# Optimization experiments

Measured on AMD Instinct MI355X. Metric: run time of the kernel, lower is better.

Reference implementation:

```python
import jax, jax.numpy as jnp
import numpy as np


def setup_inputs() -> dict:
    key = jax.random.key(0)
    k1, k2, k3 = jax.random.split(key, 3)
    N, C, Nf, W, H = 8, 256, 16, 28, 28
    l = jax.random.normal(k1, (N, C, Nf, W, H), dtype=jnp.float32)
    g = jax.random.normal(k2, (N, C, 1, 1, 1), dtype=jnp.float32)
    # 1x1x1 Conv3d(in=C, out=1, bias=False) weight collapses to a length-C vector
    w = jax.random.normal(k3, (C,), dtype=jnp.float32) * (1.0 / np.sqrt(C))
    return {"l": l, "g": g, "w": w}


def reference(l, g, w):
    # l: [N,C,Nf,W,H], g broadcastable to l, w: [C]
    N, C, Nf, W, H = l.shape
    # compatibility score: channel dot-product (1x1x1 conv, out_channels=1)
    c = jnp.einsum('ncfwh,c->nfwh', l + g, w)                      # [N,Nf,W,H]
    # softmax over the spatial dims (W*H) per frame, normalize_attn=True
    a = jax.nn.softmax(c.reshape(N, Nf, W * H), axis=-1)           # [N,Nf,WH]
    a = a.reshape(N, Nf, W, H)
    # attention-weighted spatial sum pooling -> [N,C,Nf]
    g_out = jnp.einsum('nfwh,ncfwh->ncf', a, l)
    # module returns raw compatibility map (pre-softmax) squeezed, and pooled g
    return (c, g_out)
```

## Files before the change

kernel.cpp:

```cpp
#include <hip/hip_runtime.h>
#include <math.h>

constexpr int N_ = 8, C_ = 256, F_ = 16, WH_ = 784;
constexpr int CH_STRIDE = F_ * WH_;
constexpr int COUT_SZ = N_ * F_ * WH_;
constexpr int QP = 392;
constexpr int TILE = 56;
constexpr int NT = 7;
constexpr int F4PT = TILE / 4;
constexpr int TILE_F = C_ * TILE;
constexpr int SOFF = 256 * C_;

__device__ inline float wave_reduce_sum(float v) {
#pragma unroll
  for (int o = 32; o > 0; o >>= 1) v += __shfl_down(v, o, 64);
  return v;
}

__device__ inline void gload16(const float* gp, float* lp) {
  __builtin_amdgcn_global_load_lds(
      (const __attribute__((address_space(1))) void*)gp,
      (__attribute__((address_space(3))) void*)lp, 16, 0, 0);
}

__global__ __launch_bounds__(1024, 4) void fused_kernel(
    const float* __restrict__ l, const float* __restrict__ g,
    const float* __restrict__ w, float* __restrict__ out,
    float* __restrict__ ws) {
  extern __shared__ float dbuf[];
  __shared__ float w_s[C_];
  __shared__ float e_s[TILE];
  __shared__ float red_s[16];
  __shared__ float gb_s;

  const int bid = blockIdx.x;
  const int nf = bid >> 1, half = bid & 1;
  const int n = nf >> 4, f = nf & 15;
  const int tid = threadIdx.x;
  const int lane = tid & 63, wv = tid >> 6;

  int og[4];
#pragma unroll
  for (int k = 0; k < 4; ++k) {
    const int idx = k * 1024 + tid;
    const int c = idx / F4PT, j = idx - c * F4PT;
    og[k] = c * CH_STRIDE + (j << 2);
  }
  const bool a3 = (wv < 8);
  const size_t gbase =
      (size_t)n * (C_ * CH_STRIDE) + (size_t)f * WH_ + half * QP;

  float* cur = dbuf;
  float* nxt = dbuf + TILE_F;

  {
    const float* lp = l + gbase;
    gload16(lp + og[0], &cur[wv << 8]);
    gload16(lp + og[1], &cur[4096 + (wv << 8)]);
    gload16(lp + og[2], &cur[8192 + (wv << 8)]);
    if (a3) gload16(lp + og[3], &cur[12288 + (wv << 8)]);
  }

  if (tid < C_) w_s[tid] = w[tid];
  float gv = (tid < C_) ? g[n * C_ + tid] * w[tid] : 0.f;
  gv = wave_reduce_sum(gv);
  if (lane == 0) red_s[wv] = gv;
  __syncthreads();
  if (tid == 0) {
    float s = 0.f;
#pragma unroll
    for (int i = 0; i < 16; ++i) s += red_s[i];
    gb_s = s;
  }
  __syncthreads();
  const float gb = gb_s;

  const int p16 = tid >> 4, s16 = tid & 15;
  const int gc = tid >> 2, q = tid & 3;

  float gacc = 0.f;
  float s_part = 0.f;

  for (int t = 0; t < NT; ++t) {
    if (t + 1 < NT) {
      const float* lp = l + gbase + (t + 1) * TILE;
      gload16(lp + og[0], &nxt[wv << 8]);
      gload16(lp + og[1], &nxt[4096 + (wv << 8)]);
      gload16(lp + og[2], &nxt[8192 + (wv << 8)]);
      if (a3) gload16(lp + og[3], &nxt[12288 + (wv << 8)]);
    }

    if (tid < TILE * 16) {
      float acc = 0.f;
#pragma unroll
      for (int k = 0; k < 16; ++k) {
        const int c = s16 + (k << 4);
        acc = fmaf(cur[c * TILE + p16], w_s[c], acc);
      }
      acc += __shfl_down(acc, 8, 64);
      acc += __shfl_down(acc, 4, 64);
      acc += __shfl_down(acc, 2, 64);
      acc += __shfl_down(acc, 1, 64);
      if (s16 == 0) {
        const float cp = acc + gb;
        out[nf * WH_ + half * QP + t * TILE + p16] = cp;
        const float e = __expf(cp);
        e_s[p16] = e;
        s_part += e;
      }
    }
    asm volatile("s_waitcnt lgkmcnt(0)" ::: "memory");
    __builtin_amdgcn_s_barrier();
    __builtin_amdgcn_sched_barrier(0);

    {
      const int pb = q * F4PT;
#pragma unroll
      for (int j = 0; j < 14; ++j)
        gacc = fmaf(cur[gc * TILE + pb + j], e_s[pb + j], gacc);
    }
    __syncthreads();

    float* tmp = cur; cur = nxt; nxt = tmp;
  }

  gacc += __shfl_down(gacc, 2, 64);
  gacc += __shfl_down(gacc, 1, 64);
  if (q == 0) ws[bid * C_ + gc] = gacc;

  float sp = wave_reduce_sum(s_part);
  if (lane == 0) red_s[wv] = sp;
  __syncthreads();
  if (tid == 0) {
    float ssum = 0.f;
#pragma unroll
    for (int i = 0; i < 16; ++i) ssum += red_s[i];
    ws[SOFF + bid] = ssum;
  }
}

__global__ __launch_bounds__(1024) void combine_kernel(
    float* __restrict__ out, const float* __restrict__ ws) {
  const int tg = blockIdx.x * 1024 + threadIdx.x;
  const int nf = tg >> 8, c = tg & 255;
  const int n = nf >> 4, f = nf & 15;
  const int b0 = nf << 1;
  const float G = ws[(b0 + 0) * C_ + c] + ws[(b0 + 1) * C_ + c];
  const float S = ws[SOFF + b0] + ws[SOFF + b0 + 1];
  out[COUT_SZ + (size_t)(n * C_ + c) * F_ + f] = G / S;
}

extern "C" void kernel_launch(void* const* d_in, const int* in_sizes, int n_in,
                              void* d_out, int out_size, void* d_ws,
                              size_t ws_size, hipStream_t stream) {
  const float* l = (const float*)d_in[0];
  const float* g = (const float*)d_in[1];
  const float* w = (const float*)d_in[2];
  float* out = (float*)d_out;
  float* ws = (float*)d_ws;
  fused_kernel<<<dim3(2 * N_ * F_), dim3(1024), 2 * TILE_F * sizeof(float),
                 stream>>>(l, g, w, out, ws);
  combine_kernel<<<dim3(32), dim3(1024), 0, stream>>>(out, ws);
}
```

Measured before the change: 158.1 us.

## Stage tiles through registers into padded LDS instead of direct global-to-LDS loads

Replaces the global_load_lds direct-to-LDS prefetch with register-staged float4 global loads. These are written into a padded LDS layout (row stride 60 instead of 56) after the current tile's compute. The padding aims to reduce LDS bank conflicts in the column-strided dot-product and pooling reads. In exchange it uses more registers and LDS, and adds explicit LDS store instructions. The global load latency is now hidden only by the compute that sits between the load and the store.

```diff
diff --git a/kernel.cpp b/kernel.cpp
--- a/kernel.cpp
+++ b/kernel.cpp
@@ -8,19 +8,14 @@
 constexpr int TILE = 56;
 constexpr int NT = 7;
 constexpr int F4PT = TILE / 4;
-constexpr int TILE_F = C_ * TILE;
+constexpr int LSTR = 60;
+constexpr int BUF_F = C_ * LSTR;
 constexpr int SOFF = 256 * C_;
 
 __device__ inline float wave_reduce_sum(float v) {
 #pragma unroll
   for (int o = 32; o > 0; o >>= 1) v += __shfl_down(v, o, 64);
   return v;
-}
-
-__device__ inline void gload16(const float* gp, float* lp) {
-  __builtin_amdgcn_global_load_lds(
-      (const __attribute__((address_space(1))) void*)gp,
-      (__attribute__((address_space(3))) void*)lp, 16, 0, 0);
 }
 
 __global__ __launch_bounds__(1024, 4) void fused_kernel(
@@ -39,32 +34,38 @@
   const int tid = threadIdx.x;
   const int lane = tid & 63, wv = tid >> 6;
 
-  int og[4];
-#pragma unroll
-  for (int k = 0; k < 4; ++k) {
-    const int idx = k * 1024 + tid;
-    const int c = idx / F4PT, j = idx - c * F4PT;
-    og[k] = c * CH_STRIDE + (j << 2);
-  }
-  const bool a3 = (wv < 8);
+  const int c0 = (tid) / F4PT,        j0 = (tid) - c0 * F4PT;
+  const int c1 = (1024 + tid) / F4PT, j1 = (1024 + tid) - c1 * F4PT;
+  const int c2 = (2048 + tid) / F4PT, j2 = (2048 + tid) - c2 * F4PT;
+  const int c3 = (3072 + tid) / F4PT, j3 = (3072 + tid) - c3 * F4PT;
+  const int og0 = c0 * CH_STRIDE + (j0 << 2), ol0 = c0 * LSTR + (j0 << 2);
+  const int og1 = c1 * CH_STRIDE + (j1 << 2), ol1 = c1 * LSTR + (j1 << 2);
+  const int og2 = c2 * CH_STRIDE + (j2 << 2), ol2 = c2 * LSTR + (j2 << 2);
+  const int og3 = c3 * CH_STRIDE + (j3 << 2), ol3 = c3 * LSTR + (j3 << 2);
+  const bool a3 = (tid < 512);
   const size_t gbase =
       (size_t)n * (C_ * CH_STRIDE) + (size_t)f * WH_ + half * QP;
 
   float* cur = dbuf;
-  float* nxt = dbuf + TILE_F;
+  float* nxt = dbuf + BUF_F;
 
+  float4 st0, st1, st2, st3;
   {
     const float* lp = l + gbase;
-    gload16(lp + og[0], &cur[wv << 8]);
-    gload16(lp + og[1], &cur[4096 + (wv << 8)]);
-    gload16(lp + og[2], &cur[8192 + (wv << 8)]);
-    if (a3) gload16(lp + og[3], &cur[12288 + (wv << 8)]);
+    st0 = *reinterpret_cast<const float4*>(lp + og0);
+    st1 = *reinterpret_cast<const float4*>(lp + og1);
+    st2 = *reinterpret_cast<const float4*>(lp + og2);
+    if (a3) st3 = *reinterpret_cast<const float4*>(lp + og3);
   }
 
   if (tid < C_) w_s[tid] = w[tid];
   float gv = (tid < C_) ? g[n * C_ + tid] * w[tid] : 0.f;
   gv = wave_reduce_sum(gv);
   if (lane == 0) red_s[wv] = gv;
+  *reinterpret_cast<float4*>(&cur[ol0]) = st0;
+  *reinterpret_cast<float4*>(&cur[ol1]) = st1;
+  *reinterpret_cast<float4*>(&cur[ol2]) = st2;
+  if (a3) *reinterpret_cast<float4*>(&cur[ol3]) = st3;
   __syncthreads();
   if (tid == 0) {
     float s = 0.f;
@@ -82,12 +83,13 @@
   float s_part = 0.f;
 
   for (int t = 0; t < NT; ++t) {
-    if (t + 1 < NT) {
+    const bool pf = (t + 1 < NT);
+    if (pf) {
       const float* lp = l + gbase + (t + 1) * TILE;
-      gload16(lp + og[0], &nxt[wv << 8]);
-      gload16(lp + og[1], &nxt[4096 + (wv << 8)]);
-      gload16(lp + og[2], &nxt[8192 + (wv << 8)]);
-      if (a3) gload16(lp + og[3], &nxt[12288 + (wv << 8)]);
+      st0 = *reinterpret_cast<const float4*>(lp + og0);
+      st1 = *reinterpret_cast<const float4*>(lp + og1);
+      st2 = *reinterpret_cast<const float4*>(lp + og2);
+      if (a3) st3 = *reinterpret_cast<const float4*>(lp + og3);
     }
 
     if (tid < TILE * 16) {
@@ -95,7 +97,7 @@
 #pragma unroll
       for (int k = 0; k < 16; ++k) {
         const int c = s16 + (k << 4);
-        acc = fmaf(cur[c * TILE + p16], w_s[c], acc);
+        acc = fmaf(cur[c * LSTR + p16], w_s[c], acc);
       }
       acc += __shfl_down(acc, 8, 64);
       acc += __shfl_down(acc, 4, 64);
@@ -117,7 +119,14 @@
       const int pb = q * F4PT;
 #pragma unroll
       for (int j = 0; j < 14; ++j)
-        gacc = fmaf(cur[gc * TILE + pb + j], e_s[pb + j], gacc);
+        gacc = fmaf(cur[gc * LSTR + pb + j], e_s[pb + j], gacc);
+    }
+
+    if (pf) {
+      *reinterpret_cast<float4*>(&nxt[ol0]) = st0;
+      *reinterpret_cast<float4*>(&nxt[ol1]) = st1;
+      *reinterpret_cast<float4*>(&nxt[ol2]) = st2;
+      if (a3) *reinterpret_cast<float4*>(&nxt[ol3]) = st3;
     }
     __syncthreads();
 
@@ -158,7 +167,7 @@
   const float* w = (const float*)d_in[2];
   float* out = (float*)d_out;
   float* ws = (float*)d_ws;
-  fused_kernel<<<dim3(2 * N_ * F_), dim3(1024), 2 * TILE_F * sizeof(float),
+  fused_kernel<<<dim3(2 * N_ * F_), dim3(1024), 2 * BUF_F * sizeof(float),
                  stream>>>(l, g, w, out, ws);
   combine_kernel<<<dim3(32), dim3(1024), 0, stream>>>(out, ws);
 }
```

Result: no change. 160.0 us (+1.2%).

## Triple-buffer smaller tiles with explicit vmcnt waits and deferred score stores

Applied to the files above, without the earlier changes.

Halves the tile width to 28 columns and switches from double to triple buffering, so each global-to-LDS prefetch runs two tiles ahead. Explicit vmcnt waits replace the implicit full drain, letting loads for later tiles stay in flight while the current tile is computed. Compatibility scores are kept in LDS and written to global memory once at the end instead of per tile. In exchange there are more loop iterations and barriers, and the hand-written vmcnt counts must exactly match the number of outstanding loads.

```diff
diff --git a/kernel.cpp b/kernel.cpp
--- a/kernel.cpp
+++ b/kernel.cpp
@@ -5,8 +5,8 @@
 constexpr int CH_STRIDE = F_ * WH_;
 constexpr int COUT_SZ = N_ * F_ * WH_;
 constexpr int QP = 392;
-constexpr int TILE = 56;
-constexpr int NT = 7;
+constexpr int TILE = 28;
+constexpr int NT = 14;
 constexpr int F4PT = TILE / 4;
 constexpr int TILE_F = C_ * TILE;
 constexpr int SOFF = 256 * C_;
@@ -23,6 +23,45 @@
       (__attribute__((address_space(3))) void*)lp, 16, 0, 0);
 }
 
+#define TILE_BODY(T, CUR, VMWAIT)                                            \
+  do {                                                                       \
+    if ((T) + 2 < NT && stg) {                                               \
+      const float* lp_ = l + gbase + ((T) + 2) * TILE;                       \
+      gload16(lp_ + ogA, nx2 + ldsA);                                        \
+      gload16(lp_ + ogB, nx2 + ldsB);                                        \
+    }                                                                        \
+    asm volatile(VMWAIT ::: "memory");                                       \
+    __builtin_amdgcn_s_barrier();                                            \
+    __builtin_amdgcn_sched_barrier(0);                                       \
+    if (tid < TILE * 16) {     \
+      float acc = 0.f;                                                       \
+      _Pragma("unroll") for (int k = 0; k < 16; ++k) {                       \
+        const int c_ = s16 + (k << 4);                                       \
+        acc = fmaf((CUR)[c_ * TILE + p16], w_s[c_], acc);                    \
+      }                                                                      \
+      acc += __shfl_down(acc, 8, 64);                                        \
+      acc += __shfl_down(acc, 4, 64);                                        \
+      acc += __shfl_down(acc, 2, 64);                                        \
+      acc += __shfl_down(acc, 1, 64);                                        \
+      if (s16 == 0) {                                                        \
+        const float cp = acc + gb;                                           \
+        c_save[(T) * TILE + p16] = cp;                                       \
+        const float e_ = __expf(cp);                                         \
+        e_s[p16] = e_;                                                       \
+        s_part += e_;                                                        \
+      }                                                                      \
+    }                                                                        \
+    asm volatile("s_waitcnt lgkmcnt(0)" ::: "memory");                       \
+    __builtin_amdgcn_s_barrier();                                            \
+    __builtin_amdgcn_sched_barrier(0);                                       \
+    {           \
+      _Pragma("unroll") for (int j = 0; j < F4PT; ++j)                       \
+        gacc = fmaf((CUR)[gc * TILE + pbq + j], e_s[pbq + j], gacc);         \
+    }                                                                        \
+    asm volatile("s_waitcnt lgkmcnt(0)" ::: "memory");                       \
+    __builtin_amdgcn_s_barrier();                                            \
+  } while (0)
+
 __global__ __launch_bounds__(1024, 4) void fused_kernel(
     const float* __restrict__ l, const float* __restrict__ g,
     const float* __restrict__ w, float* __restrict__ out,
@@ -30,6 +69,7 @@
   extern __shared__ float dbuf[];
   __shared__ float w_s[C_];
   __shared__ float e_s[TILE];
+  __shared__ float c_save[QP];
   __shared__ float red_s[16];
   __shared__ float gb_s;
 
@@ -39,90 +79,68 @@
   const int tid = threadIdx.x;
   const int lane = tid & 63, wv = tid >> 6;
 
-  int og[4];
-#pragma unroll
-  for (int k = 0; k < 4; ++k) {
-    const int idx = k * 1024 + tid;
-    const int c = idx / F4PT, j = idx - c * F4PT;
-    og[k] = c * CH_STRIDE + (j << 2);
-  }
-  const bool a3 = (wv < 8);
   const size_t gbase =
       (size_t)n * (C_ * CH_STRIDE) + (size_t)f * WH_ + half * QP;
 
-  float* cur = dbuf;
-  float* nxt = dbuf + TILE_F;
+  const bool stg = (tid < 896);
+  const int cA = tid / F4PT, jA = tid - cA * F4PT;
+  const int ogA = cA * CH_STRIDE + (jA << 2);
+  const int sB = 896 + tid;
+  const int cB = sB / F4PT, jB = sB - cB * F4PT;
+  const int ogB = cB * CH_STRIDE + (jB << 2);
+  const int ldsA = wv << 8;
+  const int ldsB = 3584 + (wv << 8);
 
-  {
-    const float* lp = l + gbase;
-    gload16(lp + og[0], &cur[wv << 8]);
-    gload16(lp + og[1], &cur[4096 + (wv << 8)]);
-    gload16(lp + og[2], &cur[8192 + (wv << 8)]);
-    if (a3) gload16(lp + og[3], &cur[12288 + (wv << 8)]);
+  float* b0 = dbuf;
+  float* b1 = dbuf + TILE_F;
+  float* b2 = dbuf + 2 * TILE_F;
+
+  const float wreg = (tid < C_) ? w[tid] : 0.f;
+  const float greg = (tid < C_) ? g[n * C_ + tid] : 0.f;
+  if (stg) {
+    const float* lp0 = l + gbase;
+    gload16(lp0 + ogA, b0 + ldsA);
+    gload16(lp0 + ogB, b0 + ldsB);
+    const float* lp1 = l + gbase + TILE;
+    gload16(lp1 + ogA, b1 + ldsA);
+    gload16(lp1 + ogB, b1 + ldsB);
   }
 
-  if (tid < C_) w_s[tid] = w[tid];
-  float gv = (tid < C_) ? g[n * C_ + tid] * w[tid] : 0.f;
+  if (tid < C_) w_s[tid] = wreg;
+  float gv = wreg * greg;
   gv = wave_reduce_sum(gv);
   if (lane == 0) red_s[wv] = gv;
-  __syncthreads();
+  asm volatile("s_waitcnt lgkmcnt(0)" ::: "memory");
+  __builtin_amdgcn_s_barrier();
   if (tid == 0) {
     float s = 0.f;
 #pragma unroll
     for (int i = 0; i < 16; ++i) s += red_s[i];
     gb_s = s;
   }
-  __syncthreads();
+  asm volatile("s_waitcnt lgkmcnt(0)" ::: "memory");
+  __builtin_amdgcn_s_barrier();
   const float gb = gb_s;
 
   const int p16 = tid >> 4, s16 = tid & 15;
   const int gc = tid >> 2, q = tid & 3;
+  const int pbq = q * F4PT;
 
   float gacc = 0.f;
   float s_part = 0.f;
 
-  for (int t = 0; t < NT; ++t) {
-    if (t + 1 < NT) {
-      const float* lp = l + gbase + (t + 1) * TILE;
-      gload16(lp + og[0], &nxt[wv << 8]);
-      gload16(lp + og[1], &nxt[4096 + (wv << 8)]);
-      gload16(lp + og[2], &nxt[8192 + (wv << 8)]);
-      if (a3) gload16(lp + og[3], &nxt[12288 + (wv << 8)]);
-    }
+  float* cur = b0;
+  float* nx1 = b1;
+  float* nx2 = b2;
 
-    if (tid < TILE * 16) {
-      float acc = 0.f;
-#pragma unroll
-      for (int k = 0; k < 16; ++k) {
-        const int c = s16 + (k << 4);
-        acc = fmaf(cur[c * TILE + p16], w_s[c], acc);
-      }
-      acc += __shfl_down(acc, 8, 64);
-      acc += __shfl_down(acc, 4, 64);
-      acc += __shfl_down(acc, 2, 64);
-      acc += __shfl_down(acc, 1, 64);
-      if (s16 == 0) {
-        const float cp = acc + gb;
-        out[nf * WH_ + half * QP + t * TILE + p16] = cp;
-        const float e = __expf(cp);
-        e_s[p16] = e;
-        s_part += e;
-      }
-    }
-    asm volatile("s_waitcnt lgkmcnt(0)" ::: "memory");
-    __builtin_amdgcn_s_barrier();
-    __builtin_amdgcn_sched_barrier(0);
-
-    {
-      const int pb = q * F4PT;
-#pragma unroll
-      for (int j = 0; j < 14; ++j)
-        gacc = fmaf(cur[gc * TILE + pb + j], e_s[pb + j], gacc);
-    }
-    __syncthreads();
-
-    float* tmp = cur; cur = nxt; nxt = tmp;
+#pragma unroll 1
+  for (int t = 0; t < NT - 2; ++t) {
+    TILE_BODY(t, cur, "s_waitcnt vmcnt(4)");
+    float* tmp = cur; cur = nx1; nx1 = nx2; nx2 = tmp;
   }
+  TILE_BODY(NT - 2, cur, "s_waitcnt vmcnt(2)");
+  { float* tmp = cur; cur = nx1; nx1 = nx2; nx2 = tmp; }
+  TILE_BODY(NT - 1, cur, "s_waitcnt vmcnt(0)");
 
   gacc += __shfl_down(gacc, 2, 64);
   gacc += __shfl_down(gacc, 1, 64);
@@ -137,6 +155,7 @@
     for (int i = 0; i < 16; ++i) ssum += red_s[i];
     ws[SOFF + bid] = ssum;
   }
+  if (tid < QP) out[nf * WH_ + half * QP + tid] = c_save[tid];
 }
 
 __global__ __launch_bounds__(1024) void combine_kernel(
@@ -158,7 +177,7 @@
   const float* w = (const float*)d_in[2];
   float* out = (float*)d_out;
   float* ws = (float*)d_ws;
-  fused_kernel<<<dim3(2 * N_ * F_), dim3(1024), 2 * TILE_F * sizeof(float),
+  fused_kernel<<<dim3(2 * N_ * F_), dim3(1024), 3 * TILE_F * sizeof(float),
                  stream>>>(l, g, w, out, ws);
   combine_kernel<<<dim3(32), dim3(1024), 0, stream>>>(out, ws);
 }
```

Result: no change. 158.5 us (+0.3%).
